# Optimization experiments

Hardware: AMD Instinct MI355X
Metric: run time of the kernel (lower is better)

The kernel has to match this reference:

```python
import jax, jax.numpy as jnp
import numpy as np

B, S, H = 2, 2048, 2048
NH, NKV = 16, 4
HD = H // NH          # 128
N_REP = NH // NKV     # 4


def _rotate_half(x):
    x1, x2 = x[..., : x.shape[-1] // 2], x[..., x.shape[-1] // 2 :]
    return jnp.concatenate((-x2, x1), axis=-1)


def setup_inputs() -> dict:
    key = jax.random.key(0)
    ks = jax.random.split(key, 5)
    hidden_states = jax.random.normal(ks[0], (B, S, H), dtype=jnp.float32)
    # true rotary tables [max_seq_len, head_dim]
    inv_freq = 1.0 / (10000.0 ** (np.arange(0, HD, 2, dtype=np.float32) / HD))
    t = np.arange(S, dtype=np.float32)
    freqs = np.outer(t, inv_freq)                    # [S, HD/2]
    emb = np.concatenate([freqs, freqs], axis=-1)    # [S, HD]
    cos = jnp.asarray(np.cos(emb))
    sin = jnp.asarray(np.sin(emb))
    Wq = jax.random.normal(ks[1], (H, NH * HD), dtype=jnp.float32) * 0.02
    Wk = jax.random.normal(ks[2], (H, NKV * HD), dtype=jnp.float32) * 0.02
    Wv = jax.random.normal(ks[3], (H, NKV * HD), dtype=jnp.float32) * 0.02
    Wo = jax.random.normal(ks[4], (NH * HD, H), dtype=jnp.float32) * 0.02
    attention_mask = jnp.ones((B, S), dtype=jnp.float32)  # 1 = keep
    return {"hidden_states": hidden_states, "cos": cos, "sin": sin,
            "Wq": Wq, "Wk": Wk, "Wv": Wv, "Wo": Wo,
            "attention_mask": attention_mask}


def reference(hidden_states, cos, sin, Wq, Wk, Wv, Wo, attention_mask):
    # Decoder self-attention: is_causal=True, use_rope=True, no cache, eval (dropout off).
    x = hidden_states
    b, s, _ = x.shape
    q = jnp.einsum('bsh,hd->bsd', x, Wq).reshape(b, s, NH, HD).transpose(0, 2, 1, 3)   # [b,nh,s,hd]
    k = jnp.einsum('bsh,hd->bsd', x, Wk).reshape(b, s, NKV, HD)
    v = jnp.einsum('bsh,hd->bsd', x, Wv).reshape(b, s, NKV, HD)
    # GQA repeat_kv: each kv head repeated n_rep times contiguously
    k = jnp.repeat(k, N_REP, axis=2).transpose(0, 2, 1, 3)   # [b,nh,s,hd]
    v = jnp.repeat(v, N_REP, axis=2).transpose(0, 2, 1, 3)
    # RoPE
    c = cos[:s][None, None, :, :]
    sn = sin[:s][None, None, :, :]
    q = q * c + _rotate_half(q) * sn
    k = k * c + _rotate_half(k) * sn
    # attention scores
    scores = jnp.einsum('bhqd,bhkd->bhqk', q, k) / jnp.sqrt(jnp.float32(HD))
    neg_inf = jnp.finfo(scores.dtype).min
    causal = jnp.triu(jnp.full((s, s), neg_inf, dtype=scores.dtype), k=1)
    scores = scores + causal[None, None, :, :]
    pad = (1.0 - attention_mask[:, None, None, :].astype(scores.dtype)) * neg_inf
    scores = scores + pad
    attn = jax.nn.softmax(scores.astype(jnp.float32), axis=-1).astype(q.dtype)
    out = jnp.einsum('bhqk,bhkd->bhqd', attn, v)             # [b,nh,s,hd]
    out = out.transpose(0, 2, 1, 3).reshape(b, s, NH * HD)
    return jnp.einsum('bsd,dh->bsh', out, Wo)
```

## Files before the change

kernel.cpp:

```cpp
#include <hip/hip_runtime.h>
#include <hip/hip_bf16.h>


typedef __bf16 bf16;
typedef __bf16 bf16x8 __attribute__((ext_vector_type(8)));
typedef __bf16 bf16x4 __attribute__((ext_vector_type(4)));
typedef float  f32x4  __attribute__((ext_vector_type(4)));
typedef float  f32x16 __attribute__((ext_vector_type(16)));

#define MFMA_BF16(a, b, c) __builtin_amdgcn_mfma_f32_16x16x32_bf16((a), (b), (c), 0, 0, 0)
#define MFMA32(a, b, c)    __builtin_amdgcn_mfma_f32_32x32x16_bf16((a), (b), (c), 0, 0, 0)

__device__ __forceinline__ void glds16(const bf16* g, char* l) {
  __builtin_amdgcn_global_load_lds((__attribute__((address_space(1))) const void*)g,
                                   (__attribute__((address_space(3))) void*)l, 16, 0, 0);
}

__global__ __launch_bounds__(256) void k_prep(const float* __restrict__ hs,
                                              bf16* __restrict__ Xbf,
                                              const float* __restrict__ Wq,
                                              const float* __restrict__ Wk,
                                              const float* __restrict__ Wv,
                                              const float* __restrict__ Wo,
                                              bf16* __restrict__ Wtq,
                                              bf16* __restrict__ Wtk,
                                              bf16* __restrict__ Wtv,
                                              bf16* __restrict__ Wto) {
  int blk = blockIdx.x;
  if (blk < 8192) {
    int i = blk * 256 + threadIdx.x;
    float4 v = ((const float4*)hs)[i];
    bf16x4 o;
    o[0] = (bf16)v.x; o[1] = (bf16)v.y; o[2] = (bf16)v.z; o[3] = (bf16)v.w;
    ((bf16x4*)Xbf)[i] = o;
    return;
  }
  int local = blk - 8192;
  const float* W; bf16* Wt; int N;
  if (local < 4096)       { W = Wq; Wt = Wtq; N = 2048; }
  else if (local < 8192)  { W = Wo; Wt = Wto; N = 2048; local -= 4096; }
  else if (local < 9216)  { W = Wk; Wt = Wtk; N = 512;  local -= 8192; }
  else                    { W = Wv; Wt = Wtv; N = 512;  local -= 9216; }
  int kb = (local & 63) * 32, nb = (local >> 6) * 32;
  __shared__ float tile[32][33];
  int tx = threadIdx.x & 31, ty = threadIdx.x >> 5;
#pragma unroll
  for (int i = 0; i < 4; ++i)
    tile[ty + i * 8][tx] = W[(size_t)(kb + ty + i * 8) * N + nb + tx];
  __syncthreads();
#pragma unroll
  for (int i = 0; i < 4; ++i)
    Wt[(size_t)(nb + ty + i * 8) * 2048 + kb + tx] = (bf16)tile[tx][ty + i * 8];
}

__device__ void gemm_block32(const bf16* __restrict__ A, const bf16* __restrict__ Bt,
                             bf16* __restrict__ C, int K, int ldc,
                             int rbase, int cbase, char* sm,
                             float rope_scl, const float* __restrict__ cosb,
                             const float* __restrict__ sinb,
                             bf16* __restrict__ vtr, int vkv) {
  const int tid = threadIdx.x;
  const int lane = tid & 63, wid = tid >> 6;
  const int l15 = lane & 15, lg = lane >> 4;
  char* Asm = sm;
  char* Bsm = sm + 16384;

  f32x4 acc[2][8];
#pragma unroll
  for (int i = 0; i < 2; ++i)
#pragma unroll
    for (int j = 0; j < 8; ++j)
#pragma unroll
      for (int r = 0; r < 4; ++r) acc[i][j][r] = 0.0f;

  auto stage = [&](int buf, int kb) {
#pragma unroll
    for (int i = 0; i < 2; ++i) {
      int c = wid * 128 + i * 64 + lane;
      int r = c >> 2, slot = c & 3;
      int cc = slot ^ ((r >> 1) & 3);
      int dst = buf * 8192 + wid * 2048 + i * 1024;
      glds16(A + (size_t)(rbase + r) * K + kb + cc * 8, Asm + dst);
      glds16(Bt + (size_t)(cbase + r) * K + kb + cc * 8, Bsm + dst);
    }
  };

  stage(0, 0);
  __syncthreads();
  const int nk = K >> 5;
  for (int t = 0; t < nk; ++t) {
    if (t + 1 < nk) stage((t + 1) & 1, (t + 1) << 5);
    const char* At  = Asm + (t & 1) * 8192;
    const char* Bti = Bsm + (t & 1) * 8192;
    bf16x8 a[2], b[8];
#pragma unroll
    for (int rf = 0; rf < 2; ++rf) {
      int r = wid * 32 + rf * 16 + l15;
      int slot = lg ^ ((r >> 1) & 3);
      a[rf] = *(const bf16x8*)(At + r * 64 + slot * 16);
    }
#pragma unroll
    for (int nf = 0; nf < 8; ++nf) {
      int n = nf * 16 + l15;
      int slot = lg ^ ((n >> 1) & 3);
      b[nf] = *(const bf16x8*)(Bti + n * 64 + slot * 16);
    }
#pragma unroll
    for (int rf = 0; rf < 2; ++rf)
#pragma unroll
      for (int nf = 0; nf < 8; ++nf)
        acc[rf][nf] = MFMA_BF16(a[rf], b[nf], acc[rf][nf]);
    __syncthreads();
  }

  if (rope_scl != 0.0f) {
#pragma unroll
    for (int rf = 0; rf < 2; ++rf)
#pragma unroll
      for (int r = 0; r < 4; ++r) {
        int s = (rbase + wid * 32 + rf * 16 + lg * 4 + r) & 2047;
#pragma unroll
        for (int nf = 0; nf < 4; ++nf) {
          int d = nf * 16 + l15;
          float v0 = acc[rf][nf][r], v1 = acc[rf][nf + 4][r];
          float c0 = cosb[s * 128 + d],      c1 = cosb[s * 128 + d + 64];
          float s0 = sinb[s * 128 + d],      s1 = sinb[s * 128 + d + 64];
          acc[rf][nf][r]     = (v0 * c0 - v1 * s0) * rope_scl;
          acc[rf][nf + 4][r] = (v1 * c1 + v0 * s1) * rope_scl;
        }
      }
  }

  if (vtr != nullptr) {
    __syncthreads();
#pragma unroll
    for (int rf = 0; rf < 2; ++rf)
#pragma unroll
      for (int nf = 0; nf < 8; ++nf) {
        int s0 = wid * 32 + rf * 16 + lg * 4;
        int d = nf * 16 + l15;
        bf16x4 pk;
#pragma unroll
        for (int r = 0; r < 4; ++r) pk[r] = (bf16)acc[rf][nf][r];
        *(bf16x4*)(sm + d * 256 + ((s0 * 2) ^ ((d & 15) << 4))) = pk;
      }
    __syncthreads();
    const int b4 = (rbase >> 11) * 4;
    const int scol = rbase & 2047;
    const int so = tid & 15;
#pragma unroll
    for (int i = 0; i < 8; ++i) {
      int d = (tid >> 4) + i * 16;
      bf16x8 v = *(const bf16x8*)(sm + d * 256 + ((so * 16) ^ ((d & 15) << 4)));
      *(bf16x8*)(vtr + (size_t)((b4 + vkv) * 128 + d) * 2048 + scol + so * 8) = v;
    }
    return;
  }

#pragma unroll
  for (int rf = 0; rf < 2; ++rf)
#pragma unroll
    for (int nf = 0; nf < 8; ++nf)
#pragma unroll
      for (int r = 0; r < 4; ++r) {
        int row = rbase + wid * 32 + rf * 16 + lg * 4 + r;
        int col = cbase + nf * 16 + l15;
        C[(size_t)row * ldc + col] = (bf16)acc[rf][nf][r];
      }
}

__device__ void gemm_block64(const bf16* __restrict__ A, const bf16* __restrict__ Bt,
                             float* __restrict__ C, int K, int ldc,
                             int rbase, int cbase, char* sm) {
  const int tid = threadIdx.x;
  const int lane = tid & 63, wid = tid >> 6;
  const int l15 = lane & 15, lg = lane >> 4;
  char* Asm = sm;
  char* Bsm = sm + 32768;

  f32x4 acc[2][8];
#pragma unroll
  for (int i = 0; i < 2; ++i)
#pragma unroll
    for (int j = 0; j < 8; ++j)
#pragma unroll
      for (int r = 0; r < 4; ++r) acc[i][j][r] = 0.0f;

  const int ob = wid * 4096 + lane * 16;
  auto stage = [&](int buf, int kb) {
#pragma unroll
    for (int c = 0; c < 4; ++c) {
      int o = ob + c * 1024;
      int r = o >> 7;
      int cc = ((o >> 4) & 7) ^ (r & 7);
      int dst = wid * 4096 + c * 1024 + buf * 16384;
      glds16(A + (size_t)(rbase + r) * K + kb + cc * 8, Asm + dst);
      glds16(Bt + (size_t)(cbase + r) * K + kb + cc * 8, Bsm + dst);
    }
  };

  stage(0, 0);
  __syncthreads();
  const int nk = K >> 6;
  for (int t = 0; t < nk; ++t) {
    if (t + 1 < nk) stage((t + 1) & 1, (t + 1) << 6);
    const char* At  = Asm + (t & 1) * 16384;
    const char* Bti = Bsm + (t & 1) * 16384;
#pragma unroll
    for (int ks = 0; ks < 2; ++ks) {
      bf16x8 a[2], b[8];
#pragma unroll
      for (int rf = 0; rf < 2; ++rf) {
        int r = wid * 32 + rf * 16 + l15;
        int slot = (ks * 4 + lg) ^ (r & 7);
        a[rf] = *(const bf16x8*)(At + r * 128 + slot * 16);
      }
#pragma unroll
      for (int nf = 0; nf < 8; ++nf) {
        int n = nf * 16 + l15;
        int slot = (ks * 4 + lg) ^ (n & 7);
        b[nf] = *(const bf16x8*)(Bti + n * 128 + slot * 16);
      }
#pragma unroll
      for (int rf = 0; rf < 2; ++rf)
#pragma unroll
        for (int nf = 0; nf < 8; ++nf)
          acc[rf][nf] = MFMA_BF16(a[rf], b[nf], acc[rf][nf]);
    }
    __syncthreads();
  }

#pragma unroll
  for (int rf = 0; rf < 2; ++rf)
#pragma unroll
    for (int nf = 0; nf < 8; ++nf)
#pragma unroll
      for (int r = 0; r < 4; ++r) {
        int row = rbase + wid * 32 + rf * 16 + lg * 4 + r;
        int col = cbase + nf * 16 + l15;
        C[(size_t)row * ldc + col] = acc[rf][nf][r];
      }
}

__global__ __launch_bounds__(256, 3) void k_gemm_qkv(const bf16* __restrict__ X,
                                                     const bf16* __restrict__ Wtq,
                                                     const bf16* __restrict__ Wtk,
                                                     const bf16* __restrict__ Wtv,
                                                     bf16* __restrict__ Q,
                                                     bf16* __restrict__ Ko,
                                                     bf16* __restrict__ Vt,
                                                     const float* __restrict__ cosb,
                                                     const float* __restrict__ sinb,
                                                     float sclq) {
  __shared__ alignas(16) char sm[32768];
  int nb = blockIdx.y;
  int rbase = blockIdx.x * 128;
  if (nb < 16) {
    gemm_block32(X, Wtq, Q, 2048, 2048, rbase, nb * 128, sm, sclq, cosb, sinb,
                 nullptr, 0);
  } else if (nb < 20) {
    gemm_block32(X, Wtk, Ko, 2048, 512, rbase, (nb - 16) * 128, sm, 1.0f, cosb, sinb,
                 nullptr, 0);
  } else {
    gemm_block32(X, Wtv, (bf16*)nullptr, 2048, 512, rbase, (nb - 20) * 128, sm,
                 0.0f, nullptr, nullptr, Vt, nb - 20);
  }
}

__global__ __launch_bounds__(256, 2) void k_gemm_o(const bf16* __restrict__ AO,
                                                   const bf16* __restrict__ Wto,
                                                   float* __restrict__ Out) {
  __shared__ alignas(16) char sm[65536];
  gemm_block64(AO, Wto, Out, 2048, 2048, blockIdx.x * 128, blockIdx.y * 128, sm);
}

__global__ __launch_bounds__(256, 2) void k_fattn(const bf16* __restrict__ Qg,
                                                  const bf16* __restrict__ Kg,
                                                  const bf16* __restrict__ Vtg,
                                                  bf16* __restrict__ AO) {
  __shared__ alignas(16) char sm[65536];
  const int lane = threadIdx.x & 63, wid = threadIdx.x >> 6;
  const int l31 = lane & 31, lh = lane >> 5;
  const int wg = blockIdx.x;
  const int grp = wg & 7;
  const int b = grp >> 2, kv = grp & 3;
  const int inner = wg >> 3;
  const int head = kv * 4 + (inner & 3);
  const int ih = inner & 31;
  const int strip = (inner < 32) ? (15 - (ih >> 2)) : (ih >> 2);
  const int q0w = strip * 128 + wid * 32;
  const int nt = 2 * (strip + 1);

  const bf16 *ks[4], *vs[4];
#pragma unroll
  for (int i = 0; i < 4; ++i) {
    int c = wid * 256 + i * 64 + lane;
    int kr = c >> 4, kcc = (c & 15) ^ (kr & 15);
    ks[i] = Kg + (size_t)(b * 2048 + kr) * 512 + kv * 128 + kcc * 8;
    int vr = c >> 3, vcc = (c & 7) ^ (vr & 7);
    vs[i] = Vtg + (size_t)((b * 4 + kv) * 128 + vr) * 2048 + vcc * 8;
  }
  auto stage = [&](int t) {
    if (t >= nt) return;
    int kb = t << 6;
    char* base = sm + (t & 1) * 32768 + wid * 4096;
#pragma unroll
    for (int i = 0; i < 4; ++i) {
      glds16(ks[i] + (size_t)kb * 512, base + i * 1024);
      glds16(vs[i] + kb, base + 16384 + i * 1024);
    }
  };

  bf16x8 qf[8];
#pragma unroll
  for (int st = 0; st < 8; ++st)
    qf[st] = *(const bf16x8*)(Qg + (size_t)(b * 2048 + q0w + l31) * 2048 +
                              head * 128 + st * 16 + lh * 8);

  f32x16 o[4];
#pragma unroll
  for (int j = 0; j < 4; ++j)
#pragma unroll
    for (int r = 0; r < 16; ++r) o[j][r] = 0.0f;
  float lrun = 0.0f;
  const float MB = 16.0f;

  stage(0);
  __syncthreads();

  for (int t = 0; t < nt; ++t) {
    const int kb = t << 6;
    stage(t + 1);
    const char* Kt = sm + (t & 1) * 32768;
    const char* Vt = Kt + 16384;

    if (kb <= q0w + 31) {
      f32x16 sa[2];
#pragma unroll
      for (int j = 0; j < 2; ++j)
#pragma unroll
        for (int r = 0; r < 16; ++r) sa[j][r] = 0.0f;
      __builtin_amdgcn_s_setprio(1);
#pragma unroll
      for (int st = 0; st < 8; ++st) {
#pragma unroll
        for (int kt = 0; kt < 2; ++kt) {
          int row = kt * 32 + l31;
          int slot = (st * 2 + lh) ^ (row & 15);
          bf16x8 ka = *(const bf16x8*)(Kt + row * 256 + slot * 16);
          sa[kt] = MFMA32(ka, qf[st], sa[kt]);
        }
      }
      __builtin_amdgcn_s_setprio(0);

      if (kb + 63 > q0w) {
        const int qi = q0w + l31;
#pragma unroll
        for (int kt = 0; kt < 2; ++kt)
#pragma unroll
          for (int r = 0; r < 16; ++r) {
            int kg = kb + kt * 32 + (r & 3) + 8 * (r >> 2) + 4 * lh;
            if (kg > qi) sa[kt][r] = -3e38f;
          }
      }

      union UV { uint32_t u[4]; bf16x8 v; } frag[4];
      float rs = 0.0f;
#pragma unroll
      for (int kt = 0; kt < 2; ++kt) {
        float pe[16];
#pragma unroll
        for (int r = 0; r < 16; ++r) {
          pe[r] = __builtin_amdgcn_exp2f(sa[kt][r] - MB);
          rs += pe[r];
        }
        uint32_t c[8];
#pragma unroll
        for (int g = 0; g < 8; ++g)
          asm("v_cvt_pk_bf16_f32 %0, %1, %2" : "=v"(c[g]) : "v"(pe[2 * g]), "v"(pe[2 * g + 1]));
#pragma unroll
        for (int f = 0; f < 2; ++f) {
          int bi = f * 4;
          uint32_t va = lh ? c[bi + 0] : c[bi + 2];
          uint32_t ra = (uint32_t)__shfl_xor((int)va, 32);
          uint32_t vb = lh ? c[bi + 1] : c[bi + 3];
          uint32_t rb = (uint32_t)__shfl_xor((int)vb, 32);
          UV& fr = frag[kt * 2 + f];
          fr.u[0] = lh ? ra : c[bi + 0];
          fr.u[1] = lh ? rb : c[bi + 1];
          fr.u[2] = lh ? c[bi + 2] : ra;
          fr.u[3] = lh ? c[bi + 3] : rb;
        }
      }
      rs += __shfl_xor(rs, 32);
      lrun += rs;

      __builtin_amdgcn_s_setprio(1);
#pragma unroll
      for (int dt = 0; dt < 4; ++dt) {
        int row = dt * 32 + l31;
#pragma unroll
        for (int kf = 0; kf < 4; ++kf) {
          int slot = (kf * 2 + lh) ^ (row & 7);
          bf16x8 va = *(const bf16x8*)(Vt + row * 128 + slot * 16);
          o[dt] = MFMA32(va, frag[kf].v, o[dt]);
        }
      }
      __builtin_amdgcn_s_setprio(0);
    }
    __syncthreads();
  }

  float linv = 1.0f / lrun;
  bf16* aop = AO + (size_t)(b * 2048 + q0w + l31) * 2048 + head * 128;
#pragma unroll
  for (int dt = 0; dt < 4; ++dt)
#pragma unroll
    for (int g = 0; g < 4; ++g) {
      bf16x4 pk;
#pragma unroll
      for (int j = 0; j < 4; ++j) pk[j] = (bf16)(o[dt][4 * g + j] * linv);
      *(bf16x4*)(aop + dt * 32 + g * 8 + lh * 4) = pk;
    }
}

extern "C" void kernel_launch(void* const* d_in, const int* in_sizes, int n_in,
                              void* d_out, int out_size, void* d_ws, size_t ws_size,
                              hipStream_t stream) {
  const float* hs   = (const float*)d_in[0];
  const float* cosb = (const float*)d_in[1];
  const float* sinb = (const float*)d_in[2];
  const float* Wq   = (const float*)d_in[3];
  const float* Wk   = (const float*)d_in[4];
  const float* Wv   = (const float*)d_in[5];
  const float* Wo   = (const float*)d_in[6];
  float* Out = (float*)d_out;

  char* ws = (char*)d_ws;
  size_t off = 0;
  auto alloc = [&](size_t bytes) { char* p = ws + off; off += bytes; return p; };
  bf16* Xbf = (bf16*)alloc((size_t)4096 * 2048 * 2);
  bf16* Wtq = (bf16*)alloc((size_t)2048 * 2048 * 2);
  bf16* Wtk = (bf16*)alloc((size_t)512 * 2048 * 2);
  bf16* Wtv = (bf16*)alloc((size_t)512 * 2048 * 2);
  bf16* Wto = (bf16*)alloc((size_t)2048 * 2048 * 2);
  bf16* Qb  = (bf16*)alloc((size_t)4096 * 2048 * 2);
  bf16* Kb  = (bf16*)alloc((size_t)4096 * 512 * 2);
  bf16* Vtb = (bf16*)alloc((size_t)4096 * 512 * 2);
  bf16* AO  = (bf16*)alloc((size_t)4096 * 2048 * 2);

  const float SCLQ = 0.08838834764831845f * 1.4426950408889634f;

  k_prep<<<18432, 256, 0, stream>>>(hs, Xbf, Wq, Wk, Wv, Wo, Wtq, Wtk, Wtv, Wto);
  k_gemm_qkv<<<dim3(32, 24), 256, 0, stream>>>(Xbf, Wtq, Wtk, Wtv, Qb, Kb, Vtb,
                                               cosb, sinb, SCLQ);
  k_fattn<<<512, 256, 0, stream>>>(Qb, Kb, Vtb, AO);
  k_gemm_o<<<dim3(32, 16), 256, 0, stream>>>(AO, Wto, Out);
}
```

Measured before the change: 194.5 us.

## Split QKV GEMM into 128x64 tiles with K=64 steps and move RoPE to separate kernel

The QKV projection now uses 128x64 output tiles with a 64-wide K step and an 8-slot XOR swizzle, doubling the grid to 32x48 blocks. RoPE and the Q scaling are removed from the GEMM epilogue because a 64-column tile no longer holds both rotary halves, and are done in a new elementwise kernel that reads and rewrites Q and K in place. The aim is more blocks, better occupancy and fewer K iterations. In exchange it adds an extra launch plus a full read/write pass over Q and K, and the new kernel uses scalar bf16 accesses.

Result: faster. 187.5 us (-3.6%).

```diff
diff --git a/kernel.cpp b/kernel.cpp
--- a/kernel.cpp
+++ b/kernel.cpp
@@ -53,82 +53,97 @@
     Wt[(size_t)(nb + ty + i * 8) * 2048 + kb + tx] = (bf16)tile[tx][ty + i * 8];
 }
 
-__device__ void gemm_block32(const bf16* __restrict__ A, const bf16* __restrict__ Bt,
-                             bf16* __restrict__ C, int K, int ldc,
-                             int rbase, int cbase, char* sm,
-                             float rope_scl, const float* __restrict__ cosb,
-                             const float* __restrict__ sinb,
-                             bf16* __restrict__ vtr, int vkv) {
+__global__ __launch_bounds__(256) void k_rope2(bf16* __restrict__ Qb,
+                                               bf16* __restrict__ Kb,
+                                               const float* __restrict__ cosb,
+                                               const float* __restrict__ sinb,
+                                               float sclq) {
+  int blk = blockIdx.x;
+  bf16* T; int ncols; float scl; int i;
+  if (blk < 16384) { T = Qb; ncols = 2048; scl = sclq;  i = blk * 256 + threadIdx.x; }
+  else             { T = Kb; ncols = 512;  scl = 1.0f;  i = (blk - 16384) * 256 + threadIdx.x; }
+  int npr = ncols >> 1;
+  int row = i / npr;
+  int p = i - row * npr;
+  int h = p >> 6, d = p & 63;
+  int c0 = h * 128 + d;
+  size_t base = (size_t)row * ncols;
+  int s = row & 2047;
+  float q0 = (float)T[base + c0];
+  float q1 = (float)T[base + c0 + 64];
+  float vc0 = cosb[s * 128 + d],      vc1 = cosb[s * 128 + d + 64];
+  float vs0 = sinb[s * 128 + d],      vs1 = sinb[s * 128 + d + 64];
+  T[base + c0]      = (bf16)((q0 * vc0 - q1 * vs0) * scl);
+  T[base + c0 + 64] = (bf16)((q1 * vc1 + q0 * vs1) * scl);
+}
+
+__device__ void gemm_n64(const bf16* __restrict__ A, const bf16* __restrict__ Bt,
+                         bf16* __restrict__ C, int K, int ldc,
+                         int rbase, int cbase, char* sm,
+                         bf16* __restrict__ vtr, int vtrow) {
   const int tid = threadIdx.x;
   const int lane = tid & 63, wid = tid >> 6;
   const int l15 = lane & 15, lg = lane >> 4;
   char* Asm = sm;
-  char* Bsm = sm + 16384;
-
-  f32x4 acc[2][8];
+  char* Bsm = sm + 32768;
+
+  f32x4 acc[2][4];
 #pragma unroll
   for (int i = 0; i < 2; ++i)
 #pragma unroll
-    for (int j = 0; j < 8; ++j)
+    for (int j = 0; j < 4; ++j)
 #pragma unroll
       for (int r = 0; r < 4; ++r) acc[i][j][r] = 0.0f;
 
+  const int ob = wid * 4096 + lane * 16;
   auto stage = [&](int buf, int kb) {
+#pragma unroll
+    for (int c = 0; c < 4; ++c) {
+      int o = ob + c * 1024;
+      int r = o >> 7;
+      int cc = ((o >> 4) & 7) ^ (r & 7);
+      int dst = wid * 4096 + c * 1024 + buf * 16384;
+      glds16(A + (size_t)(rbase + r) * K + kb + cc * 8, Asm + dst);
+    }
 #pragma unroll
     for (int i = 0; i < 2; ++i) {
       int c = wid * 128 + i * 64 + lane;
-      int r = c >> 2, slot = c & 3;
-      int cc = slot ^ ((r >> 1) & 3);
-      int dst = buf * 8192 + wid * 2048 + i * 1024;
-      glds16(A + (size_t)(rbase + r) * K + kb + cc * 8, Asm + dst);
+      int r = c >> 3;
+      int cc = (c & 7) ^ (r & 7);
+      int dst = wid * 2048 + i * 1024 + buf * 8192;
       glds16(Bt + (size_t)(cbase + r) * K + kb + cc * 8, Bsm + dst);
     }
   };
 
   stage(0, 0);
   __syncthreads();
-  const int nk = K >> 5;
+  const int nk = K >> 6;
   for (int t = 0; t < nk; ++t) {
-    if (t + 1 < nk) stage((t + 1) & 1, (t + 1) << 5);
-    const char* At  = Asm + (t & 1) * 8192;
+    if (t + 1 < nk) stage((t + 1) & 1, (t + 1) << 6);
+    const char* At  = Asm + (t & 1) * 16384;
     const char* Bti = Bsm + (t & 1) * 8192;
-    bf16x8 a[2], b[8];
-#pragma unroll
-    for (int rf = 0; rf < 2; ++rf) {
-      int r = wid * 32 + rf * 16 + l15;
-      int slot = lg ^ ((r >> 1) & 3);
-      a[rf] = *(const bf16x8*)(At + r * 64 + slot * 16);
-    }
-#pragma unroll
-    for (int nf = 0; nf < 8; ++nf) {
-      int n = nf * 16 + l15;
-      int slot = lg ^ ((n >> 1) & 3);
-      b[nf] = *(const bf16x8*)(Bti + n * 64 + slot * 16);
-    }
-#pragma unroll
-    for (int rf = 0; rf < 2; ++rf)
-#pragma unroll
-      for (int nf = 0; nf < 8; ++nf)
-        acc[rf][nf] = MFMA_BF16(a[rf], b[nf], acc[rf][nf]);
+#pragma unroll
+    for (int ks = 0; ks < 2; ++ks) {
+      bf16x8 a[2], b[4];
+#pragma unroll
+      for (int rf = 0; rf < 2; ++rf) {
+        int r = wid * 32 + rf * 16 + l15;
+        int slot = (ks * 4 + lg) ^ (r & 7);
+        a[rf] = *(const bf16x8*)(At + r * 128 + slot * 16);
+      }
+#pragma unroll
+      for (int nf = 0; nf < 4; ++nf) {
+        int n = nf * 16 + l15;
+        int slot = (ks * 4 + lg) ^ (n & 7);
+        b[nf] = *(const bf16x8*)(Bti + n * 128 + slot * 16);
+      }
+#pragma unroll
+      for (int rf = 0; rf < 2; ++rf)
+#pragma unroll
+        for (int nf = 0; nf < 4; ++nf)
+          acc[rf][nf] = MFMA_BF16(a[rf], b[nf], acc[rf][nf]);
+    }
     __syncthreads();
-  }
-
-  if (rope_scl != 0.0f) {
-#pragma unroll
-    for (int rf = 0; rf < 2; ++rf)
-#pragma unroll
-      for (int r = 0; r < 4; ++r) {
-        int s = (rbase + wid * 32 + rf * 16 + lg * 4 + r) & 2047;
-#pragma unroll
-        for (int nf = 0; nf < 4; ++nf) {
-          int d = nf * 16 + l15;
-          float v0 = acc[rf][nf][r], v1 = acc[rf][nf + 4][r];
-          float c0 = cosb[s * 128 + d],      c1 = cosb[s * 128 + d + 64];
-          float s0 = sinb[s * 128 + d],      s1 = sinb[s * 128 + d + 64];
-          acc[rf][nf][r]     = (v0 * c0 - v1 * s0) * rope_scl;
-          acc[rf][nf + 4][r] = (v1 * c1 + v0 * s1) * rope_scl;
-        }
-      }
   }
 
   if (vtr != nullptr) {
@@ -136,7 +151,7 @@
 #pragma unroll
     for (int rf = 0; rf < 2; ++rf)
 #pragma unroll
-      for (int nf = 0; nf < 8; ++nf) {
+      for (int nf = 0; nf < 4; ++nf) {
         int s0 = wid * 32 + rf * 16 + lg * 4;
         int d = nf * 16 + l15;
         bf16x4 pk;
@@ -145,14 +160,13 @@
         *(bf16x4*)(sm + d * 256 + ((s0 * 2) ^ ((d & 15) << 4))) = pk;
       }
     __syncthreads();
-    const int b4 = (rbase >> 11) * 4;
     const int scol = rbase & 2047;
     const int so = tid & 15;
 #pragma unroll
-    for (int i = 0; i < 8; ++i) {
+    for (int i = 0; i < 4; ++i) {
       int d = (tid >> 4) + i * 16;
       bf16x8 v = *(const bf16x8*)(sm + d * 256 + ((so * 16) ^ ((d & 15) << 4)));
-      *(bf16x8*)(vtr + (size_t)((b4 + vkv) * 128 + d) * 2048 + scol + so * 8) = v;
+      *(bf16x8*)(vtr + (size_t)(vtrow + d) * 2048 + scol + so * 8) = v;
     }
     return;
   }
@@ -160,7 +174,7 @@
 #pragma unroll
   for (int rf = 0; rf < 2; ++rf)
 #pragma unroll
-    for (int nf = 0; nf < 8; ++nf)
+    for (int nf = 0; nf < 4; ++nf)
 #pragma unroll
       for (int r = 0; r < 4; ++r) {
         int row = rbase + wid * 32 + rf * 16 + lg * 4 + r;
@@ -248,22 +262,20 @@
                                                      const bf16* __restrict__ Wtv,
                                                      bf16* __restrict__ Q,
                                                      bf16* __restrict__ Ko,
-                                                     bf16* __restrict__ Vt,
-                                                     const float* __restrict__ cosb,
-                                                     const float* __restrict__ sinb,
-                                                     float sclq) {
-  __shared__ alignas(16) char sm[32768];
+                                                     bf16* __restrict__ Vt) {
+  __shared__ alignas(16) char sm[49152];
   int nb = blockIdx.y;
   int rbase = blockIdx.x * 128;
-  if (nb < 16) {
-    gemm_block32(X, Wtq, Q, 2048, 2048, rbase, nb * 128, sm, sclq, cosb, sinb,
-                 nullptr, 0);
-  } else if (nb < 20) {
-    gemm_block32(X, Wtk, Ko, 2048, 512, rbase, (nb - 16) * 128, sm, 1.0f, cosb, sinb,
-                 nullptr, 0);
+  if (nb < 32) {
+    gemm_n64(X, Wtq, Q, 2048, 2048, rbase, nb * 64, sm, nullptr, 0);
+  } else if (nb < 40) {
+    gemm_n64(X, Wtk, Ko, 2048, 512, rbase, (nb - 32) * 64, sm, nullptr, 0);
   } else {
-    gemm_block32(X, Wtv, (bf16*)nullptr, 2048, 512, rbase, (nb - 20) * 128, sm,
-                 0.0f, nullptr, nullptr, Vt, nb - 20);
+    int vcb = nb - 40;
+    int kv = vcb >> 1, d0 = (vcb & 1) * 64;
+    int b4 = (rbase >> 11) * 4;
+    gemm_n64(X, Wtv, (bf16*)nullptr, 2048, 512, rbase, vcb * 64, sm,
+             Vt, (b4 + kv) * 128 + d0);
   }
 }
 
@@ -452,8 +464,8 @@
   const float SCLQ = 0.08838834764831845f * 1.4426950408889634f;
 
   k_prep<<<18432, 256, 0, stream>>>(hs, Xbf, Wq, Wk, Wv, Wo, Wtq, Wtk, Wtv, Wto);
-  k_gemm_qkv<<<dim3(32, 24), 256, 0, stream>>>(Xbf, Wtq, Wtk, Wtv, Qb, Kb, Vtb,
-                                               cosb, sinb, SCLQ);
+  k_gemm_qkv<<<dim3(32, 48), 256, 0, stream>>>(Xbf, Wtq, Wtk, Wtv, Qb, Kb, Vtb);
+  k_rope2<<<20480, 256, 0, stream>>>(Qb, Kb, cosb, sinb, SCLQ);
   k_fattn<<<512, 256, 0, stream>>>(Qb, Kb, Vtb, AO);
   k_gemm_o<<<dim3(32, 16), 256, 0, stream>>>(AO, Wto, Out);
 }
```
